# Performance work log

Measured on AMD Instinct MI355X. Metric: run time of the kernel, lower is better.

The kernel has to match this reference:

```python
import jax, jax.numpy as jnp
import numpy as np

B, N_ANT, M_MEAS, D_A, MAX_ITER = 1024, 64, 16, 4096, 20
SC_L = 10


def setup_inputs() -> dict:
    key = jax.random.key(0)
    ks = jax.random.split(key, 9)
    return {
        "x_re": jax.random.normal(ks[0], (B, M_MEAS), jnp.float32),
        "x_im": jax.random.normal(ks[1], (B, M_MEAS), jnp.float32),
        "xm_re": jax.random.normal(ks[2], (B, N_ANT), jnp.float32),
        "xm_im": jax.random.normal(ks[3], (B, N_ANT), jnp.float32),
        "M_re": jax.random.normal(ks[4], (B, N_ANT, M_MEAS), jnp.float32),
        "M_im": jax.random.normal(ks[5], (B, N_ANT, M_MEAS), jnp.float32),
        "W_re": jax.random.normal(ks[6], (N_ANT, D_A), jnp.float32),
        "W_im": jax.random.normal(ks[7], (N_ANT, D_A), jnp.float32),
        "sigma": jax.random.uniform(ks[8], (B,), jnp.float32) * 0.05,
        "L": SC_L,
        "k": 1,
    }


def _mpnet_forward(x, xm, M, W, sigma, L):
    # M_D[b] = conj(M[b]^T) @ W  -> [B, m, d_a]
    M_D = jnp.einsum('bnm,na->bma', jnp.conj(M), W)
    # per-sample column normalization (norms are constants: torch computes them on detached numpy)
    md_norm = jax.lax.stop_gradient(
        jnp.sqrt(jnp.sum(jnp.abs(M_D) ** 2, axis=1, keepdims=True)))  # [B,1,d_a]
    M_D = M_D / md_norm
    e_norm = jax.lax.stop_gradient(
        jnp.sqrt(jnp.sum(jnp.abs(W) ** 2, axis=0, keepdims=True)))  # [1,d_a]
    E = W / e_norm  # [N, d_a]

    n_full = xm.shape[1]
    threshold = (sigma ** 2) * n_full * L  # sc == 2

    def body(carry, _):
        residual, res, active = carry
        rn2 = jnp.sum(jnp.abs(residual) ** 2, axis=1)         # [B]
        active = active & (rn2 >= threshold)                  # per-sample early exit
        corr = jnp.einsum('bm,bma->ba', residual, jnp.conj(M_D))  # [B,d_a]
        idx = jnp.argmax(jnp.abs(corr), axis=1)               # top-1 (keep_k_max, k=1)
        val = jnp.take_along_axis(corr, idx[:, None], axis=1)           # [B,1]
        col = jnp.take_along_axis(M_D, idx[:, None, None], axis=2)[..., 0]  # [B,m]
        colE = jnp.take(E, idx, axis=1).T                     # [B,N]
        residual = jnp.where(active[:, None], residual - val * col, residual)
        res = jnp.where(active[:, None], res - val * colE, res)
        return (residual, res, active), None

    init = (x, xm, jnp.ones((x.shape[0],), dtype=bool))
    (residual, res, _), _ = jax.lax.scan(body, init, None, length=MAX_ITER)
    x_hat = x - residual
    x_hat_m = xm - res
    return residual, x_hat, x_hat_m


def reference(x_re, x_im, xm_re, xm_im, M_re, M_im, W_re, W_im, sigma, L, k):
    x = (x_re + 1j * x_im).astype(jnp.complex64)
    xm = (xm_re + 1j * xm_im).astype(jnp.complex64)
    M = (M_re + 1j * M_im).astype(jnp.complex64)
    W = (W_re + 1j * W_im).astype(jnp.complex64)
    return _mpnet_forward(x, xm, M, W, sigma, L)
```

## Files before the change

### kernel.cpp

```cpp
#include <hip/hip_runtime.h>
#include <cstdint>
#include <cstddef>

#define NB_TOT 1024
#define NANT 64
#define MM 16
#define MPAD 17
#define DA 4096
#define MAXIT 20
#define SPB 4
#define NTHR 1024
#define JCOLS 4
#define L_CONST 10.0f
#define MD_BYTES ((size_t)NB_TOT * DA * sizeof(float))

__global__ __launch_bounds__(256, 8)
void md_kernel(const float* __restrict__ M_re, const float* __restrict__ M_im,
               const float* __restrict__ W_re, const float* __restrict__ W_im,
               float* __restrict__ md_ws)
{
  const int b   = blockIdx.x >> 1;
  const int h   = blockIdx.x & 1;
  const int tid = threadIdx.x;
  const float* MrS = M_re + (size_t)b*1024;
  const float* MiS = M_im + (size_t)b*1024;

  #pragma unroll
  for (int k = 0; k < 8; k++){
    const int col = h*2048 + k*256 + tid;
    float cr[MM], ci[MM];
    #pragma unroll
    for (int q = 0; q < MM; q++){ cr[q]=0.f; ci[q]=0.f; }
    #pragma unroll 2
    for (int n = 0; n < NANT; n++){
      float wr = W_re[(size_t)n*DA + col];
      float wi = W_im[(size_t)n*DA + col];
      const float* Mr = MrS + n*MM;
      const float* Mi = MiS + n*MM;
      #pragma unroll
      for (int q2 = 0; q2 < 4; q2++){
        float4 m4r = *(const float4*)(Mr + q2*4);
        float4 m4i = *(const float4*)(Mi + q2*4);
        cr[q2*4+0] += m4r.x*wr + m4i.x*wi;  ci[q2*4+0] += m4r.x*wi - m4i.x*wr;
        cr[q2*4+1] += m4r.y*wr + m4i.y*wi;  ci[q2*4+1] += m4r.y*wi - m4i.y*wr;
        cr[q2*4+2] += m4r.z*wr + m4i.z*wi;  ci[q2*4+2] += m4r.z*wi - m4i.z*wr;
        cr[q2*4+3] += m4r.w*wr + m4i.w*wi;  ci[q2*4+3] += m4r.w*wi - m4i.w*wr;
      }
    }
    float nrm = 0.f;
    #pragma unroll
    for (int q = 0; q < MM; q++) nrm += cr[q]*cr[q] + ci[q]*ci[q];
    md_ws[(size_t)b*DA + col] = 1.f/sqrtf(nrm);
  }
}

__global__ __launch_bounds__(NTHR, 4)
void loop_kernel(const float* __restrict__ x_re, const float* __restrict__ x_im,
                 const float* __restrict__ xm_re, const float* __restrict__ xm_im,
                 const float* __restrict__ M_re, const float* __restrict__ M_im,
                 const float* __restrict__ W_re, const float* __restrict__ W_im,
                 const float* __restrict__ sigma, const float* __restrict__ md_ws,
                 float* __restrict__ out, int outn_i)
{
  __shared__ float Msh_re[SPB][NANT][MPAD];
  __shared__ float Msh_im[SPB][NANT][MPAD];
  __shared__ float tsh[NANT][8];
  __shared__ float rsd_re[SPB][MM], rsd_im[SPB][MM];
  __shared__ float resh_re[SPB][NANT], resh_im[SPB][NANT];
  __shared__ float red_c2[16][SPB];
  __shared__ int   red_ix[16][SPB];
  __shared__ float rn2_sh[SPB], thr_sh[SPB];
  __shared__ int   actsh[SPB];

  const int tid = threadIdx.x;
  const int b0 = blockIdx.x * SPB;
  const size_t outn = (size_t)outn_i;

  for (int k2 = 0; k2 < 4; k2++){
    int idx = k2*NTHR + tid;
    int s = idx >> 10, rem = idx & 1023;
    int n = rem >> 4, m = rem & 15;
    Msh_re[s][n][m] = M_re[(size_t)b0*1024 + idx];
    Msh_im[s][n][m] = M_im[(size_t)b0*1024 + idx];
  }
  if (tid < SPB*MM){
    int s = tid >> 4, m = tid & 15;
    rsd_re[s][m] = x_re[(b0+s)*MM + m];
    rsd_im[s][m] = x_im[(b0+s)*MM + m];
  } else if (tid >= 64 && tid < 64 + SPB*NANT){
    int q = tid - 64, s = q >> 6, n = q & 63;
    resh_re[s][n] = xm_re[(b0+s)*NANT + n];
    resh_im[s][n] = xm_im[(b0+s)*NANT + n];
  } else if (tid >= 448 && tid < 448 + SPB){
    int s = tid - 448;
    float sg = sigma[b0+s];
    thr_sh[s] = ((sg*sg) * (float)NANT) * L_CONST;
    actsh[s] = 1;
  }
  __syncthreads();

  for (int it = 0; it < MAXIT; it++){
    if (tid < SPB){
      float e = 0.f;
      #pragma unroll
      for (int m = 0; m < MM; m++){
        float rr = rsd_re[tid][m], ri = rsd_im[tid][m];
        e += rr*rr + ri*ri;
      }
      rn2_sh[tid] = e;
    } else if (tid >= 64 && tid < 320){
      int q = tid - 64, s = q >> 6, n = q & 63;
      if (actsh[s]){
        float tr = 0.f, ti = 0.f;
        #pragma unroll
        for (int m = 0; m < MM; m++){
          float mr = Msh_re[s][n][m], mi = Msh_im[s][n][m];
          float rr = rsd_re[s][m], ri = rsd_im[s][m];
          tr += mr*rr - mi*ri;
          ti += mr*ri + mi*rr;
        }
        tsh[n][2*s]   = tr;
        tsh[n][2*s+1] = ti;
      }
    }
    __syncthreads();

    bool a0 = actsh[0] && (rn2_sh[0] >= thr_sh[0]);
    bool a1 = actsh[1] && (rn2_sh[1] >= thr_sh[1]);
    bool a2 = actsh[2] && (rn2_sh[2] >= thr_sh[2]);
    bool a3 = actsh[3] && (rn2_sh[3] >= thr_sh[3]);
    if (tid < 4){
      int v = (tid==0) ? (int)a0 : (tid==1) ? (int)a1 : (tid==2) ? (int)a2 : (int)a3;
      actsh[tid] = v;
    }
    if (!(a0 || a1 || a2 || a3)) break;

    float gr[SPB][JCOLS], gi[SPB][JCOLS];
    #pragma unroll
    for (int s = 0; s < SPB; s++)
      #pragma unroll
      for (int j = 0; j < JCOLS; j++){ gr[s][j]=0.f; gi[s][j]=0.f; }
    #pragma unroll 8
    for (int n = 0; n < NANT; n++){
      float4 t01 = *(const float4*)&tsh[n][0];
      float4 t23 = *(const float4*)&tsh[n][4];
      float4 wr = *(const float4*)(W_re + (size_t)n*DA + (tid<<2));
      float4 wi = *(const float4*)(W_im + (size_t)n*DA + (tid<<2));
      if (a0){
        gr[0][0] += wr.x*t01.x + wi.x*t01.y;  gi[0][0] += wr.x*t01.y - wi.x*t01.x;
        gr[0][1] += wr.y*t01.x + wi.y*t01.y;  gi[0][1] += wr.y*t01.y - wi.y*t01.x;
        gr[0][2] += wr.z*t01.x + wi.z*t01.y;  gi[0][2] += wr.z*t01.y - wi.z*t01.x;
        gr[0][3] += wr.w*t01.x + wi.w*t01.y;  gi[0][3] += wr.w*t01.y - wi.w*t01.x;
      }
      if (a1){
        gr[1][0] += wr.x*t01.z + wi.x*t01.w;  gi[1][0] += wr.x*t01.w - wi.x*t01.z;
        gr[1][1] += wr.y*t01.z + wi.y*t01.w;  gi[1][1] += wr.y*t01.w - wi.y*t01.z;
        gr[1][2] += wr.z*t01.z + wi.z*t01.w;  gi[1][2] += wr.z*t01.w - wi.z*t01.z;
        gr[1][3] += wr.w*t01.z + wi.w*t01.w;  gi[1][3] += wr.w*t01.w - wi.w*t01.z;
      }
      if (a2){
        gr[2][0] += wr.x*t23.x + wi.x*t23.y;  gi[2][0] += wr.x*t23.y - wi.x*t23.x;
        gr[2][1] += wr.y*t23.x + wi.y*t23.y;  gi[2][1] += wr.y*t23.y - wi.y*t23.x;
        gr[2][2] += wr.z*t23.x + wi.z*t23.y;  gi[2][2] += wr.z*t23.y - wi.z*t23.x;
        gr[2][3] += wr.w*t23.x + wi.w*t23.y;  gi[2][3] += wr.w*t23.y - wi.w*t23.x;
      }
      if (a3){
        gr[3][0] += wr.x*t23.z + wi.x*t23.w;  gi[3][0] += wr.x*t23.w - wi.x*t23.z;
        gr[3][1] += wr.y*t23.z + wi.y*t23.w;  gi[3][1] += wr.y*t23.w - wi.y*t23.z;
        gr[3][2] += wr.z*t23.z + wi.z*t23.w;  gi[3][2] += wr.z*t23.w - wi.z*t23.z;
        gr[3][3] += wr.w*t23.z + wi.w*t23.w;  gi[3][3] += wr.w*t23.w - wi.w*t23.z;
      }
    }

    const bool acts[4] = {a0, a1, a2, a3};
    float bc2[SPB]; int bix[SPB];
    #pragma unroll
    for (int s = 0; s < SPB; s++){
      bc2[s] = -1.f; bix[s] = 0;
      if (acts[s]){
        float4 md4 = *(const float4*)(md_ws + (size_t)(b0+s)*DA + (tid<<2));
        float c0 = (gr[s][0]*gr[s][0] + gi[s][0]*gi[s][0]) * (md4.x*md4.x);
        float c1 = (gr[s][1]*gr[s][1] + gi[s][1]*gi[s][1]) * (md4.y*md4.y);
        float c2v = (gr[s][2]*gr[s][2] + gi[s][2]*gi[s][2]) * (md4.z*md4.z);
        float c3 = (gr[s][3]*gr[s][3] + gi[s][3]*gi[s][3]) * (md4.w*md4.w);
        float bc = c0; int bi = (tid<<2);
        if (c1 > bc){ bc = c1; bi = (tid<<2)+1; }
        if (c2v > bc){ bc = c2v; bi = (tid<<2)+2; }
        if (c3 > bc){ bc = c3; bi = (tid<<2)+3; }
        bc2[s] = bc; bix[s] = bi;
      }
    }
    #pragma unroll
    for (int s = 0; s < SPB; s++){
      if (acts[s]){
        #pragma unroll
        for (int off = 32; off; off >>= 1){
          float oc2 = __shfl_down(bc2[s], off);
          int   oix = __shfl_down(bix[s], off);
          if (oc2 > bc2[s] || (oc2 == bc2[s] && oix < bix[s])){ bc2[s]=oc2; bix[s]=oix; }
        }
      }
    }
    if ((tid & 63) == 0){
      int wid = tid >> 6;
      #pragma unroll
      for (int s = 0; s < SPB; s++){
        if (acts[s]){ red_c2[wid][s]=bc2[s]; red_ix[wid][s]=bix[s]; }
      }
    }
    __syncthreads();

    if (tid < 256){
      int s = tid >> 6, lane = tid & 63;
      if (actsh[s]){
        float c = (lane < 16) ? red_c2[lane][s] : -1.f;
        int   bi = (lane < 16) ? red_ix[lane][s] : 0x7FFFFFFF;
        #pragma unroll
        for (int off = 8; off; off >>= 1){
          float oc = __shfl_xor(c, off);
          int   oi = __shfl_xor(bi, off);
          if (oc > c || (oc == c && oi < bi)){ c = oc; bi = oi; }
        }
        int I = __shfl(bi, 0);
        float wr = W_re[(size_t)lane*DA + I], wi = W_im[(size_t)lane*DA + I];
        float tr = tsh[lane][2*s], ti = tsh[lane][2*s+1];
        float vr = wr*tr + wi*ti;
        float vi = wr*ti - wi*tr;
        float w2 = wr*wr + wi*wi;
        #pragma unroll
        for (int off = 32; off; off >>= 1){
          vr += __shfl_xor(vr, off);
          vi += __shfl_xor(vi, off);
          w2 += __shfl_xor(w2, off);
        }
        float mdv = md_ws[(size_t)(b0+s)*DA + I];
        float val_r = vr*mdv, val_i = vi*mdv;
        float einv = rsqrtf(w2);
        float er = wr*einv, em = wi*einv;
        resh_re[s][lane] -= val_r*er - val_i*em;
        resh_im[s][lane] -= val_r*em + val_i*er;
        for (int m = 0; m < MM; m++){
          float mr = Msh_re[s][lane][m], mi = Msh_im[s][lane][m];
          float pr = mr*wr + mi*wi;
          float pi = mr*wi - mi*wr;
          #pragma unroll
          for (int off = 32; off; off >>= 1){
            pr += __shfl_xor(pr, off);
            pi += __shfl_xor(pi, off);
          }
          if (lane == m){
            float col_r = pr*mdv, col_i = pi*mdv;
            rsd_re[s][m] -= val_r*col_r - val_i*col_i;
            rsd_im[s][m] -= val_r*col_i + val_i*col_r;
          }
        }
      }
    }
    __syncthreads();
  }

  if (tid < 64){
    int s = tid >> 4, m = tid & 15; int b = b0 + s;
    float rr = rsd_re[s][m], ri = rsd_im[s][m];
    size_t base = (size_t)b*MM + m;
    if (base < outn)          out[base]          = rr;
    if (16384 + base < outn)  out[16384 + base]  = x_re[b*MM+m] - rr;
    if (98304 + base < outn)  out[98304 + base]  = ri;
    if (114688 + base < outn) out[114688 + base] = x_im[b*MM+m] - ri;
  } else if (tid >= 64 && tid < 320){
    int q = tid - 64, s = q >> 6, n = q & 63; int b = b0 + s;
    size_t base = (size_t)b*NANT + n;
    if (32768 + base < outn)  out[32768 + base]  = xm_re[b*NANT+n] - resh_re[s][n];
    if (131072 + base < outn) out[131072 + base] = xm_im[b*NANT+n] - resh_im[s][n];
  }
}

__global__ __launch_bounds__(NTHR, 4)
void fused_kernel(const float* __restrict__ x_re, const float* __restrict__ x_im,
                  const float* __restrict__ xm_re, const float* __restrict__ xm_im,
                  const float* __restrict__ M_re, const float* __restrict__ M_im,
                  const float* __restrict__ W_re, const float* __restrict__ W_im,
                  const float* __restrict__ sigma,
                  float* __restrict__ out, int outn_i)
{
  __shared__ float Msh_re[SPB][NANT][MPAD];
  __shared__ float Msh_im[SPB][NANT][MPAD];
  __shared__ float md_T[SPB][JCOLS][NTHR];
  __shared__ float tsh[NANT][8];
  __shared__ float rsd_re[SPB][MM], rsd_im[SPB][MM];
  __shared__ float resh_re[SPB][NANT], resh_im[SPB][NANT];
  __shared__ float red_c2[16][SPB];
  __shared__ int   red_ix[16][SPB];
  __shared__ float rn2_sh[SPB], thr_sh[SPB];
  __shared__ int   actsh[SPB];

  const int tid = threadIdx.x;
  const int b0 = blockIdx.x * SPB;
  const size_t outn = (size_t)outn_i;

  for (int k2 = 0; k2 < 4; k2++){
    int idx = k2*NTHR + tid;
    int s = idx >> 10, rem = idx & 1023;
    int n = rem >> 4, m = rem & 15;
    Msh_re[s][n][m] = M_re[(size_t)b0*1024 + idx];
    Msh_im[s][n][m] = M_im[(size_t)b0*1024 + idx];
  }
  if (tid < SPB*MM){
    int s = tid >> 4, m = tid & 15;
    rsd_re[s][m] = x_re[(b0+s)*MM + m];
    rsd_im[s][m] = x_im[(b0+s)*MM + m];
  } else if (tid >= 64 && tid < 64 + SPB*NANT){
    int q = tid - 64, s = q >> 6, n = q & 63;
    resh_re[s][n] = xm_re[(b0+s)*NANT + n];
    resh_im[s][n] = xm_im[(b0+s)*NANT + n];
  } else if (tid >= 448 && tid < 448 + SPB){
    int s = tid - 448;
    float sg = sigma[b0+s];
    thr_sh[s] = ((sg*sg) * (float)NANT) * L_CONST;
    actsh[s] = 1;
  }

  #pragma unroll
  for (int s = 0; s < SPB; s++){
    const float* MrS = M_re + (size_t)(b0+s)*1024;
    const float* MiS = M_im + (size_t)(b0+s)*1024;
    #pragma unroll
    for (int jc = 0; jc < JCOLS; jc++){
      const int col = (tid<<2) + jc;
      float cr[MM], ci[MM];
      #pragma unroll
      for (int q = 0; q < MM; q++){ cr[q]=0.f; ci[q]=0.f; }
      #pragma unroll 2
      for (int n = 0; n < NANT; n++){
        float wr = W_re[(size_t)n*DA + col];
        float wi = W_im[(size_t)n*DA + col];
        const float* Mr = MrS + n*MM;
        const float* Mi = MiS + n*MM;
        #pragma unroll
        for (int q2 = 0; q2 < 4; q2++){
          float4 m4r = *(const float4*)(Mr + q2*4);
          float4 m4i = *(const float4*)(Mi + q2*4);
          cr[q2*4+0] += m4r.x*wr + m4i.x*wi;  ci[q2*4+0] += m4r.x*wi - m4i.x*wr;
          cr[q2*4+1] += m4r.y*wr + m4i.y*wi;  ci[q2*4+1] += m4r.y*wi - m4i.y*wr;
          cr[q2*4+2] += m4r.z*wr + m4i.z*wi;  ci[q2*4+2] += m4r.z*wi - m4i.z*wr;
          cr[q2*4+3] += m4r.w*wr + m4i.w*wi;  ci[q2*4+3] += m4r.w*wi - m4i.w*wr;
        }
      }
      float nrm = 0.f;
      #pragma unroll
      for (int q = 0; q < MM; q++) nrm += cr[q]*cr[q] + ci[q]*ci[q];
      md_T[s][jc][tid] = 1.f/sqrtf(nrm);
    }
  }
  __syncthreads();

  for (int it = 0; it < MAXIT; it++){
    if (tid < SPB){
      float e = 0.f;
      #pragma unroll
      for (int m = 0; m < MM; m++){
        float rr = rsd_re[tid][m], ri = rsd_im[tid][m];
        e += rr*rr + ri*ri;
      }
      rn2_sh[tid] = e;
    } else if (tid >= 64 && tid < 320){
      int q = tid - 64, s = q >> 6, n = q & 63;
      if (actsh[s]){
        float tr = 0.f, ti = 0.f;
        #pragma unroll
        for (int m = 0; m < MM; m++){
          float mr = Msh_re[s][n][m], mi = Msh_im[s][n][m];
          float rr = rsd_re[s][m], ri = rsd_im[s][m];
          tr += mr*rr - mi*ri;
          ti += mr*ri + mi*rr;
        }
        tsh[n][2*s]   = tr;
        tsh[n][2*s+1] = ti;
      }
    }
    __syncthreads();

    bool a0 = actsh[0] && (rn2_sh[0] >= thr_sh[0]);
    bool a1 = actsh[1] && (rn2_sh[1] >= thr_sh[1]);
    bool a2 = actsh[2] && (rn2_sh[2] >= thr_sh[2]);
    bool a3 = actsh[3] && (rn2_sh[3] >= thr_sh[3]);
    if (tid < 4){
      int v = (tid==0) ? (int)a0 : (tid==1) ? (int)a1 : (tid==2) ? (int)a2 : (int)a3;
      actsh[tid] = v;
    }
    if (!(a0 || a1 || a2 || a3)) break;

    float gr[SPB][JCOLS], gi[SPB][JCOLS];
    #pragma unroll
    for (int s = 0; s < SPB; s++)
      #pragma unroll
      for (int j = 0; j < JCOLS; j++){ gr[s][j]=0.f; gi[s][j]=0.f; }
    #pragma unroll 8
    for (int n = 0; n < NANT; n++){
      float4 t01 = *(const float4*)&tsh[n][0];
      float4 t23 = *(const float4*)&tsh[n][4];
      float4 wr = *(const float4*)(W_re + (size_t)n*DA + (tid<<2));
      float4 wi = *(const float4*)(W_im + (size_t)n*DA + (tid<<2));
      if (a0){
        gr[0][0] += wr.x*t01.x + wi.x*t01.y;  gi[0][0] += wr.x*t01.y - wi.x*t01.x;
        gr[0][1] += wr.y*t01.x + wi.y*t01.y;  gi[0][1] += wr.y*t01.y - wi.y*t01.x;
        gr[0][2] += wr.z*t01.x + wi.z*t01.y;  gi[0][2] += wr.z*t01.y - wi.z*t01.x;
        gr[0][3] += wr.w*t01.x + wi.w*t01.y;  gi[0][3] += wr.w*t01.y - wi.w*t01.x;
      }
      if (a1){
        gr[1][0] += wr.x*t01.z + wi.x*t01.w;  gi[1][0] += wr.x*t01.w - wi.x*t01.z;
        gr[1][1] += wr.y*t01.z + wi.y*t01.w;  gi[1][1] += wr.y*t01.w - wi.y*t01.z;
        gr[1][2] += wr.z*t01.z + wi.z*t01.w;  gi[1][2] += wr.z*t01.w - wi.z*t01.z;
        gr[1][3] += wr.w*t01.z + wi.w*t01.w;  gi[1][3] += wr.w*t01.w - wi.w*t01.z;
      }
      if (a2){
        gr[2][0] += wr.x*t23.x + wi.x*t23.y;  gi[2][0] += wr.x*t23.y - wi.x*t23.x;
        gr[2][1] += wr.y*t23.x + wi.y*t23.y;  gi[2][1] += wr.y*t23.y - wi.y*t23.x;
        gr[2][2] += wr.z*t23.x + wi.z*t23.y;  gi[2][2] += wr.z*t23.y - wi.z*t23.x;
        gr[2][3] += wr.w*t23.x + wi.w*t23.y;  gi[2][3] += wr.w*t23.y - wi.w*t23.x;
      }
      if (a3){
        gr[3][0] += wr.x*t23.z + wi.x*t23.w;  gi[3][0] += wr.x*t23.w - wi.x*t23.z;
        gr[3][1] += wr.y*t23.z + wi.y*t23.w;  gi[3][1] += wr.y*t23.w - wi.y*t23.z;
        gr[3][2] += wr.z*t23.z + wi.z*t23.w;  gi[3][2] += wr.z*t23.w - wi.z*t23.z;
        gr[3][3] += wr.w*t23.z + wi.w*t23.w;  gi[3][3] += wr.w*t23.w - wi.w*t23.z;
      }
    }

    const bool acts[4] = {a0, a1, a2, a3};
    float bc2[SPB]; int bix[SPB];
    #pragma unroll
    for (int s = 0; s < SPB; s++){
      bc2[s] = -1.f; bix[s] = 0;
      if (acts[s]){
        float m0 = md_T[s][0][tid], m1 = md_T[s][1][tid];
        float m2 = md_T[s][2][tid], m3 = md_T[s][3][tid];
        float c0 = (gr[s][0]*gr[s][0] + gi[s][0]*gi[s][0]) * (m0*m0);
        float c1 = (gr[s][1]*gr[s][1] + gi[s][1]*gi[s][1]) * (m1*m1);
        float c2v = (gr[s][2]*gr[s][2] + gi[s][2]*gi[s][2]) * (m2*m2);
        float c3 = (gr[s][3]*gr[s][3] + gi[s][3]*gi[s][3]) * (m3*m3);
        float bc = c0; int bi = (tid<<2);
        if (c1 > bc){ bc = c1; bi = (tid<<2)+1; }
        if (c2v > bc){ bc = c2v; bi = (tid<<2)+2; }
        if (c3 > bc){ bc = c3; bi = (tid<<2)+3; }
        bc2[s] = bc; bix[s] = bi;
      }
    }
    #pragma unroll
    for (int s = 0; s < SPB; s++){
      if (acts[s]){
        #pragma unroll
        for (int off = 32; off; off >>= 1){
          float oc2 = __shfl_down(bc2[s], off);
          int   oix = __shfl_down(bix[s], off);
          if (oc2 > bc2[s] || (oc2 == bc2[s] && oix < bix[s])){ bc2[s]=oc2; bix[s]=oix; }
        }
      }
    }
    if ((tid & 63) == 0){
      int wid = tid >> 6;
      #pragma unroll
      for (int s = 0; s < SPB; s++){
        if (acts[s]){ red_c2[wid][s]=bc2[s]; red_ix[wid][s]=bix[s]; }
      }
    }
    __syncthreads();

    if (tid < 256){
      int s = tid >> 6, lane = tid & 63;
      if (actsh[s]){
        float c = (lane < 16) ? red_c2[lane][s] : -1.f;
        int   bi = (lane < 16) ? red_ix[lane][s] : 0x7FFFFFFF;
        #pragma unroll
        for (int off = 8; off; off >>= 1){
          float oc = __shfl_xor(c, off);
          int   oi = __shfl_xor(bi, off);
          if (oc > c || (oc == c && oi < bi)){ c = oc; bi = oi; }
        }
        int I = __shfl(bi, 0);
        float wr = W_re[(size_t)lane*DA + I], wi = W_im[(size_t)lane*DA + I];
        float tr = tsh[lane][2*s], ti = tsh[lane][2*s+1];
        float vr = wr*tr + wi*ti;
        float vi = wr*ti - wi*tr;
        float w2 = wr*wr + wi*wi;
        #pragma unroll
        for (int off = 32; off; off >>= 1){
          vr += __shfl_xor(vr, off);
          vi += __shfl_xor(vi, off);
          w2 += __shfl_xor(w2, off);
        }
        float mdv = md_T[s][I & 3][I >> 2];
        float val_r = vr*mdv, val_i = vi*mdv;
        float einv = rsqrtf(w2);
        float er = wr*einv, em = wi*einv;
        resh_re[s][lane] -= val_r*er - val_i*em;
        resh_im[s][lane] -= val_r*em + val_i*er;
        for (int m = 0; m < MM; m++){
          float mr = Msh_re[s][lane][m], mi = Msh_im[s][lane][m];
          float pr = mr*wr + mi*wi;
          float pi = mr*wi - mi*wr;
          #pragma unroll
          for (int off = 32; off; off >>= 1){
            pr += __shfl_xor(pr, off);
            pi += __shfl_xor(pi, off);
          }
          if (lane == m){
            float col_r = pr*mdv, col_i = pi*mdv;
            rsd_re[s][m] -= val_r*col_r - val_i*col_i;
            rsd_im[s][m] -= val_r*col_i + val_i*col_r;
          }
        }
      }
    }
    __syncthreads();
  }

  if (tid < 64){
    int s = tid >> 4, m = tid & 15; int b = b0 + s;
    float rr = rsd_re[s][m], ri = rsd_im[s][m];
    size_t base = (size_t)b*MM + m;
    if (base < outn)          out[base]          = rr;
    if (16384 + base < outn)  out[16384 + base]  = x_re[b*MM+m] - rr;
    if (98304 + base < outn)  out[98304 + base]  = ri;
    if (114688 + base < outn) out[114688 + base] = x_im[b*MM+m] - ri;
  } else if (tid >= 64 && tid < 320){
    int q = tid - 64, s = q >> 6, n = q & 63; int b = b0 + s;
    size_t base = (size_t)b*NANT + n;
    if (32768 + base < outn)  out[32768 + base]  = xm_re[b*NANT+n] - resh_re[s][n];
    if (131072 + base < outn) out[131072 + base] = xm_im[b*NANT+n] - resh_im[s][n];
  }
}

extern "C" void kernel_launch(void* const* d_in, const int* in_sizes, int n_in,
                              void* d_out, int out_size, void* d_ws, size_t ws_size,
                              hipStream_t stream) {
  (void)in_sizes; (void)n_in;
  const float* x_re  = (const float*)d_in[0];
  const float* x_im  = (const float*)d_in[1];
  const float* xm_re = (const float*)d_in[2];
  const float* xm_im = (const float*)d_in[3];
  const float* M_re  = (const float*)d_in[4];
  const float* M_im  = (const float*)d_in[5];
  const float* W_re  = (const float*)d_in[6];
  const float* W_im  = (const float*)d_in[7];
  const float* sig   = (const float*)d_in[8];
  float* out = (float*)d_out;

  if (ws_size >= MD_BYTES && d_ws != nullptr){
    float* md_ws = (float*)d_ws;
    hipLaunchKernelGGL(md_kernel, dim3(2048), dim3(256), 0, stream,
                       M_re, M_im, W_re, W_im, md_ws);
    hipLaunchKernelGGL(loop_kernel, dim3(NB_TOT / SPB), dim3(NTHR), 0, stream,
                       x_re, x_im, xm_re, xm_im, M_re, M_im, W_re, W_im,
                       sig, md_ws, out, out_size);
  } else {
    hipLaunchKernelGGL(fused_kernel, dim3(NB_TOT / SPB), dim3(NTHR), 0, stream,
                       x_re, x_im, xm_re, xm_im, M_re, M_im, W_re, W_im,
                       sig, out, out_size);
  }
}
```

Measured before the change: 1.436 ms.

## Parallelize residual column update across threads instead of serial shuffle reductions

The per-iteration update that rebuilt the selected dictionary column used a serial loop of 16 full-wavefront shuffle reductions per sample. It now stages the selected W column and scalars in shared memory. A separate phase then spreads the work over 512 threads (one per sample, measurement and 8-antenna group, with short 8-lane reductions) and 256 further threads handle the antenna-domain residual. The argmax reduction also uses width-16 shuffles. This adds an extra block-wide barrier per iteration and more shared memory.

After: 1.376 ms. -4.2%, faster.

```diff
diff --git a/kernel.cpp b/kernel.cpp
--- a/kernel.cpp
+++ b/kernel.cpp
@@ -69,6 +69,9 @@
   __shared__ float resh_re[SPB][NANT], resh_im[SPB][NANT];
   __shared__ float red_c2[16][SPB];
   __shared__ int   red_ix[16][SPB];
+  __shared__ float wselr[SPB][NANT], wseli[SPB][NANT];
+  __shared__ int   sel_ix[SPB];
+  __shared__ float sel_vr[SPB], sel_vi[SPB], sel_md[SPB], sel_ei[SPB];
   __shared__ float rn2_sh[SPB], thr_sh[SPB];
   __shared__ int   actsh[SPB];
 
@@ -217,12 +220,14 @@
         int   bi = (lane < 16) ? red_ix[lane][s] : 0x7FFFFFFF;
         #pragma unroll
         for (int off = 8; off; off >>= 1){
-          float oc = __shfl_xor(c, off);
-          int   oi = __shfl_xor(bi, off);
+          float oc = __shfl_xor(c, off, 16);
+          int   oi = __shfl_xor(bi, off, 16);
           if (oc > c || (oc == c && oi < bi)){ c = oc; bi = oi; }
         }
         int I = __shfl(bi, 0);
         float wr = W_re[(size_t)lane*DA + I], wi = W_im[(size_t)lane*DA + I];
+        wselr[s][lane] = wr;
+        wseli[s][lane] = wi;
         float tr = tsh[lane][2*s], ti = tsh[lane][2*s+1];
         float vr = wr*tr + wi*ti;
         float vi = wr*ti - wi*tr;
@@ -233,27 +238,48 @@
           vi += __shfl_xor(vi, off);
           w2 += __shfl_xor(w2, off);
         }
-        float mdv = md_ws[(size_t)(b0+s)*DA + I];
-        float val_r = vr*mdv, val_i = vi*mdv;
-        float einv = rsqrtf(w2);
-        float er = wr*einv, em = wi*einv;
-        resh_re[s][lane] -= val_r*er - val_i*em;
-        resh_im[s][lane] -= val_r*em + val_i*er;
-        for (int m = 0; m < MM; m++){
-          float mr = Msh_re[s][lane][m], mi = Msh_im[s][lane][m];
-          float pr = mr*wr + mi*wi;
-          float pi = mr*wi - mi*wr;
-          #pragma unroll
-          for (int off = 32; off; off >>= 1){
-            pr += __shfl_xor(pr, off);
-            pi += __shfl_xor(pi, off);
-          }
-          if (lane == m){
-            float col_r = pr*mdv, col_i = pi*mdv;
-            rsd_re[s][m] -= val_r*col_r - val_i*col_i;
-            rsd_im[s][m] -= val_r*col_i + val_i*col_r;
-          }
-        }
+        if (lane == 0){
+          float mdv = md_ws[(size_t)(b0+s)*DA + I];
+          sel_ix[s] = I;
+          sel_vr[s] = vr*mdv;
+          sel_vi[s] = vi*mdv;
+          sel_md[s] = mdv;
+          sel_ei[s] = rsqrtf(w2);
+        }
+      }
+    }
+    __syncthreads();
+
+    if (tid < 512){
+      int s = tid >> 7, rem = tid & 127, m = rem >> 3, g = rem & 7;
+      if (actsh[s]){
+        float pr = 0.f, pi = 0.f;
+        #pragma unroll
+        for (int j = 0; j < 8; j++){
+          int n = g*8 + j;
+          float mr = Msh_re[s][n][m], mi = Msh_im[s][n][m];
+          float wr = wselr[s][n],     wi = wseli[s][n];
+          pr += mr*wr + mi*wi;
+          pi += mr*wi - mi*wr;
+        }
+        pr += __shfl_xor(pr, 4, 8);  pi += __shfl_xor(pi, 4, 8);
+        pr += __shfl_xor(pr, 2, 8);  pi += __shfl_xor(pi, 2, 8);
+        pr += __shfl_xor(pr, 1, 8);  pi += __shfl_xor(pi, 1, 8);
+        if (g == 0){
+          float mdv = sel_md[s], vr = sel_vr[s], vi = sel_vi[s];
+          float cr = pr*mdv, ci2 = pi*mdv;
+          rsd_re[s][m] -= vr*cr - vi*ci2;
+          rsd_im[s][m] -= vr*ci2 + vi*cr;
+        }
+      }
+    } else if (tid < 768){
+      int q = tid - 512, s = q >> 6, n = q & 63;
+      if (actsh[s]){
+        float wr = wselr[s][n], wi = wseli[s][n];
+        float ei = sel_ei[s], vr = sel_vr[s], vi = sel_vi[s];
+        float er = wr*ei, em = wi*ei;
+        resh_re[s][n] -= vr*er - vi*em;
+        resh_im[s][n] -= vr*em + vi*er;
       }
     }
     __syncthreads();
```
